# Optimization experiments

Hardware: AMD Instinct MI355X
Metric: run time of the kernel (lower is better)

## Reference

```python
import jax, jax.numpy as jnp
import numpy as np

# Bit index 0 = LSB of the IEEE-754 uint32 pattern (little-endian bit order):
# bits[..., 0:23] mantissa, bits[..., 23:31] exponent, bits[..., 31] sign.
_SHIFTS = jnp.arange(32, dtype=jnp.uint32)


def f32_to_bits(x):
    """float32 [...] -> pulse bits [..., 32] in {0., 1.}."""
    u = jax.lax.bitcast_convert_type(x, jnp.uint32)
    return ((u[..., None] >> _SHIFTS) & jnp.uint32(1)).astype(jnp.float32)


def bits_to_f32(b):
    """pulse bits [..., 32] -> float32 [...]. Exact inverse of f32_to_bits."""
    u = jnp.sum(b.astype(jnp.uint32) << _SHIFTS, axis=-1, dtype=jnp.uint32)
    return jax.lax.bitcast_convert_type(u, jnp.float32)


def setup_inputs() -> dict:
    key = jax.random.key(0)
    kA, kB = jax.random.split(key)
    # Encode realistic fp32 values into pulse (bit) tensors.
    A_vals = jax.random.normal(kA, (4, 512, 512), dtype=jnp.float32)   # [B, M, K]
    B_vals = jax.random.normal(kB, (512, 512), dtype=jnp.float32)      # [K, N]
    return {"A": f32_to_bits(A_vals), "B": f32_to_bits(B_vals)}


def reference(A, B):
    """Spike-domain FP32 matmul: decode pulses -> fp32 GEMM -> re-encode pulses.

    A: [..., M, K, 32] pulses, B: [K, N, 32] pulses -> C: [..., M, N, 32] pulses.
    The spiking multiplier/adder gates implement exact IEEE-754 fp32 multiply
    and sequential accumulation over k, i.e. C[..., i, j] = sum_k A[...,i,k]*B[k,j]
    in fp32.
    """
    A_f = bits_to_f32(A)                         # [B, M, K]
    B_f = bits_to_f32(B)                         # [K, N]
    C = jnp.einsum('bmk,kn->bmn', A_f, B_f)      # fp32 accumulation
    return f32_to_bits(C)                        # [B, M, N, 32]
```

## Files before the change

### kernel.cpp

```cpp
#include <hip/hip_runtime.h>
#include <stdint.h>

#define BATCH 4
#define MDIM  512
#define KDIM  512
#define NDIM  512
#define ROWS  (BATCH * MDIM)
#define BR    4
#define BCOLS 256

#define WORDS_A (ROWS * KDIM)
#define WORDS_B (KDIM * NDIM)
#define WORDS_T (WORDS_A + WORDS_B)
#define DEC_BLOCKS 2048
#define DEC_WAVES  (DEC_BLOCKS * 4)
#define DEC_ITERS  (WORDS_T / (32 * DEC_WAVES))

__device__ __forceinline__ uint32_t spread4(uint32_t x) {
    x = (x | (x << 12)) & 0x000F000Fu;
    x = (x | (x << 6))  & 0x03030303u;
    x = (x | (x << 3))  & 0x11111111u;
    return x;
}

__global__ __launch_bounds__(256) void decode_all(const float* __restrict__ Abits,
                                                  const float* __restrict__ Bbits,
                                                  uint32_t* __restrict__ Au,
                                                  uint32_t* __restrict__ Bu) {
    const int lane = threadIdx.x & 63;
    const int waveId = (blockIdx.x * blockDim.x + threadIdx.x) >> 6;
    const int sh = lane & 56;

#pragma unroll
    for (int i = 0; i < DEC_ITERS; ++i) {
        const int wb = (waveId + i * DEC_WAVES) * 32;
        const float* src;
        uint32_t* dst;
        if (wb < WORDS_A) { src = Abits + (size_t)wb * 32;             dst = Au + wb; }
        else              { src = Bbits + (size_t)(wb - WORDS_A) * 32; dst = Bu + (wb - WORDS_A); }

        uint4 v0 = ((const uint4*)src)[lane];
        uint4 v1 = ((const uint4*)src)[lane + 64];
        uint4 v2 = ((const uint4*)src)[lane + 128];
        uint4 v3 = ((const uint4*)src)[lane + 192];

        unsigned long long m[16];
        m[0]  = __ballot((v0.x >> 29) & 1u);
        m[1]  = __ballot((v0.y >> 29) & 1u);
        m[2]  = __ballot((v0.z >> 29) & 1u);
        m[3]  = __ballot((v0.w >> 29) & 1u);
        m[4]  = __ballot((v1.x >> 29) & 1u);
        m[5]  = __ballot((v1.y >> 29) & 1u);
        m[6]  = __ballot((v1.z >> 29) & 1u);
        m[7]  = __ballot((v1.w >> 29) & 1u);
        m[8]  = __ballot((v2.x >> 29) & 1u);
        m[9]  = __ballot((v2.y >> 29) & 1u);
        m[10] = __ballot((v2.z >> 29) & 1u);
        m[11] = __ballot((v2.w >> 29) & 1u);
        m[12] = __ballot((v3.x >> 29) & 1u);
        m[13] = __ballot((v3.y >> 29) & 1u);
        m[14] = __ballot((v3.z >> 29) & 1u);
        m[15] = __ballot((v3.w >> 29) & 1u);

        if ((lane & 7) == 0) {
#pragma unroll
            for (int g = 0; g < 4; ++g) {
                uint32_t w = (spread4((uint32_t)(m[4*g+0] >> sh) & 0xFFu) << 0)
                           | (spread4((uint32_t)(m[4*g+1] >> sh) & 0xFFu) << 1)
                           | (spread4((uint32_t)(m[4*g+2] >> sh) & 0xFFu) << 2)
                           | (spread4((uint32_t)(m[4*g+3] >> sh) & 0xFFu) << 3);
                dst[8 * g + (lane >> 3)] = w;
            }
        }
    }
}

__global__ __launch_bounds__(256) void gemm_encode(const float* __restrict__ A,
                                                   const float* __restrict__ B,
                                                   float* __restrict__ outbits) {
    __shared__ uint32_t Us[BR][BCOLS];

    const int tid = threadIdx.x;
    const int rowBase = blockIdx.x * BR;
    const int n0 = blockIdx.y * BCOLS;
    const int n = n0 + tid;

    float acc[BR];
#pragma unroll
    for (int r = 0; r < BR; ++r) acc[r] = 0.0f;

    const float* Bcol = B + n;
    const float* Arow = A + (size_t)rowBase * KDIM;

    float bn[8], bc[8];
#pragma unroll
    for (int i = 0; i < 8; ++i) bn[i] = Bcol[(size_t)i * NDIM];

#pragma unroll 2
    for (int k0 = 0; k0 < KDIM; k0 += 8) {
#pragma unroll
        for (int i = 0; i < 8; ++i) bc[i] = bn[i];
        const int kp = (k0 + 8) & (KDIM - 1);
#pragma unroll
        for (int i = 0; i < 8; ++i) bn[i] = Bcol[(size_t)(kp + i) * NDIM];

        float4 a0[BR], a1[BR];
#pragma unroll
        for (int r = 0; r < BR; ++r) {
            a0[r] = *(const float4*)(Arow + (size_t)r * KDIM + k0);
            a1[r] = *(const float4*)(Arow + (size_t)r * KDIM + k0 + 4);
        }
#pragma unroll
        for (int r = 0; r < BR; ++r) {
            acc[r] = __builtin_fmaf(a0[r].x, bc[0], acc[r]);
            acc[r] = __builtin_fmaf(a0[r].y, bc[1], acc[r]);
            acc[r] = __builtin_fmaf(a0[r].z, bc[2], acc[r]);
            acc[r] = __builtin_fmaf(a0[r].w, bc[3], acc[r]);
            acc[r] = __builtin_fmaf(a1[r].x, bc[4], acc[r]);
            acc[r] = __builtin_fmaf(a1[r].y, bc[5], acc[r]);
            acc[r] = __builtin_fmaf(a1[r].z, bc[6], acc[r]);
            acc[r] = __builtin_fmaf(a1[r].w, bc[7], acc[r]);
        }
    }

#pragma unroll
    for (int r = 0; r < BR; ++r) Us[r][tid] = __float_as_uint(acc[r]);
    __syncthreads();

    float* oBase = outbits + ((size_t)rowBase * NDIM + n0) * 32;
    const int b = (tid & 7) * 4;
#pragma unroll
    for (int r = 0; r < BR; ++r) {
        float* o = oBase + (size_t)r * NDIM * 32;
#pragma unroll
        for (int it = 0; it < 8; ++it) {
            uint32_t u = Us[r][it * 32 + (tid >> 3)];
            float4 q;
            q.x = (float)((u >> (b + 0)) & 1u);
            q.y = (float)((u >> (b + 1)) & 1u);
            q.z = (float)((u >> (b + 2)) & 1u);
            q.w = (float)((u >> (b + 3)) & 1u);
            *(float4*)(o + it * 1024 + tid * 4) = q;
        }
    }
}

extern "C" void kernel_launch(void* const* d_in, const int* in_sizes, int n_in,
                              void* d_out, int out_size, void* d_ws, size_t ws_size,
                              hipStream_t stream) {
    const float* Abits = (const float*)d_in[0];
    const float* Bbits = (const float*)d_in[1];
    float* out = (float*)d_out;

    uint32_t* A_u = (uint32_t*)d_ws;
    uint32_t* B_u = A_u + WORDS_A;

    decode_all<<<DEC_BLOCKS, 256, 0, stream>>>(Abits, Bbits, A_u, B_u);

    dim3 grid(ROWS / BR, NDIM / BCOLS);
    gemm_encode<<<grid, 256, 0, stream>>>((const float*)A_u, (const float*)B_u, out);
}
```

Measured before the change: 83.84 us.

## Fuse A pulse decoding into GEMM kernel via shared memory, widen block to full N

The decode of A's bit tensor moves into the GEMM kernel. Each 512-thread block decodes its 4-row A panel straight into shared memory and then computes all 512 output columns. This removes the round trip of writing the decoded A words to global memory and reading them back, and A is decoded once per row panel rather than being read by two column blocks. Only B is still decoded by a separate kernel. The cost is fewer blocks (512 instead of 1024) and a decode phase inside each block that has to finish before the FMA loop can start.

```diff
diff --git a/kernel.cpp b/kernel.cpp
--- a/kernel.cpp
+++ b/kernel.cpp
@@ -7,14 +7,9 @@
 #define NDIM  512
 #define ROWS  (BATCH * MDIM)
 #define BR    4
-#define BCOLS 256
+#define THREADS 512
 
-#define WORDS_A (ROWS * KDIM)
 #define WORDS_B (KDIM * NDIM)
-#define WORDS_T (WORDS_A + WORDS_B)
-#define DEC_BLOCKS 2048
-#define DEC_WAVES  (DEC_BLOCKS * 4)
-#define DEC_ITERS  (WORDS_T / (32 * DEC_WAVES))
 
 __device__ __forceinline__ uint32_t spread4(uint32_t x) {
     x = (x | (x << 12)) & 0x000F000Fu;
@@ -23,74 +18,93 @@
     return x;
 }
 
-__global__ __launch_bounds__(256) void decode_all(const float* __restrict__ Abits,
-                                                  const float* __restrict__ Bbits,
-                                                  uint32_t* __restrict__ Au,
-                                                  uint32_t* __restrict__ Bu) {
+__global__ __launch_bounds__(256) void decode_B(const float* __restrict__ Bbits,
+                                                uint32_t* __restrict__ Bu) {
     const int lane = threadIdx.x & 63;
     const int waveId = (blockIdx.x * blockDim.x + threadIdx.x) >> 6;
     const int sh = lane & 56;
 
+    const int wb = waveId * 32;
+    const float* src = Bbits + (size_t)wb * 32;
+    uint32_t* dst = Bu + wb;
+
+    uint4 v0 = ((const uint4*)src)[lane];
+    uint4 v1 = ((const uint4*)src)[lane + 64];
+    uint4 v2 = ((const uint4*)src)[lane + 128];
+    uint4 v3 = ((const uint4*)src)[lane + 192];
+
+    unsigned long long m[16];
+    m[0]  = __ballot((v0.x >> 29) & 1u);  m[1]  = __ballot((v0.y >> 29) & 1u);
+    m[2]  = __ballot((v0.z >> 29) & 1u);  m[3]  = __ballot((v0.w >> 29) & 1u);
+    m[4]  = __ballot((v1.x >> 29) & 1u);  m[5]  = __ballot((v1.y >> 29) & 1u);
+    m[6]  = __ballot((v1.z >> 29) & 1u);  m[7]  = __ballot((v1.w >> 29) & 1u);
+    m[8]  = __ballot((v2.x >> 29) & 1u);  m[9]  = __ballot((v2.y >> 29) & 1u);
+    m[10] = __ballot((v2.z >> 29) & 1u);  m[11] = __ballot((v2.w >> 29) & 1u);
+    m[12] = __ballot((v3.x >> 29) & 1u);  m[13] = __ballot((v3.y >> 29) & 1u);
+    m[14] = __ballot((v3.z >> 29) & 1u);  m[15] = __ballot((v3.w >> 29) & 1u);
+
+    if ((lane & 7) == 0) {
 #pragma unroll
-    for (int i = 0; i < DEC_ITERS; ++i) {
-        const int wb = (waveId + i * DEC_WAVES) * 32;
-        const float* src;
-        uint32_t* dst;
-        if (wb < WORDS_A) { src = Abits + (size_t)wb * 32;             dst = Au + wb; }
-        else              { src = Bbits + (size_t)(wb - WORDS_A) * 32; dst = Bu + (wb - WORDS_A); }
+        for (int q = 0; q < 4; ++q) {
+            uint32_t w = (spread4((uint32_t)(m[4*q+0] >> sh) & 0xFFu) << 0)
+                       | (spread4((uint32_t)(m[4*q+1] >> sh) & 0xFFu) << 1)
+                       | (spread4((uint32_t)(m[4*q+2] >> sh) & 0xFFu) << 2)
+                       | (spread4((uint32_t)(m[4*q+3] >> sh) & 0xFFu) << 3);
+            dst[8 * q + (lane >> 3)] = w;
+        }
+    }
+}
 
+__global__ __launch_bounds__(THREADS) void gemm_fused(const float* __restrict__ Abits,
+                                                      const float* __restrict__ Bu,
+                                                      float* __restrict__ outbits) {
+    __shared__ uint32_t AsU[BR][KDIM];
+
+    const int tid  = threadIdx.x;
+    const int lane = tid & 63;
+    const int wv   = tid >> 6;
+    const int rowBase = blockIdx.x * BR;
+    const int sh = lane & 56;
+
+    const float* panel = Abits + (size_t)rowBase * KDIM * 32;
+#pragma unroll
+    for (int i = 0; i < 8; ++i) {
+        const float* src = panel + wv * 8192 + i * 1024;
         uint4 v0 = ((const uint4*)src)[lane];
         uint4 v1 = ((const uint4*)src)[lane + 64];
         uint4 v2 = ((const uint4*)src)[lane + 128];
         uint4 v3 = ((const uint4*)src)[lane + 192];
 
         unsigned long long m[16];
-        m[0]  = __ballot((v0.x >> 29) & 1u);
-        m[1]  = __ballot((v0.y >> 29) & 1u);
-        m[2]  = __ballot((v0.z >> 29) & 1u);
-        m[3]  = __ballot((v0.w >> 29) & 1u);
-        m[4]  = __ballot((v1.x >> 29) & 1u);
-        m[5]  = __ballot((v1.y >> 29) & 1u);
-        m[6]  = __ballot((v1.z >> 29) & 1u);
-        m[7]  = __ballot((v1.w >> 29) & 1u);
-        m[8]  = __ballot((v2.x >> 29) & 1u);
-        m[9]  = __ballot((v2.y >> 29) & 1u);
-        m[10] = __ballot((v2.z >> 29) & 1u);
-        m[11] = __ballot((v2.w >> 29) & 1u);
-        m[12] = __ballot((v3.x >> 29) & 1u);
-        m[13] = __ballot((v3.y >> 29) & 1u);
-        m[14] = __ballot((v3.z >> 29) & 1u);
-        m[15] = __ballot((v3.w >> 29) & 1u);
+        m[0]  = __ballot((v0.x >> 29) & 1u);  m[1]  = __ballot((v0.y >> 29) & 1u);
+        m[2]  = __ballot((v0.z >> 29) & 1u);  m[3]  = __ballot((v0.w >> 29) & 1u);
+        m[4]  = __ballot((v1.x >> 29) & 1u);  m[5]  = __ballot((v1.y >> 29) & 1u);
+        m[6]  = __ballot((v1.z >> 29) & 1u);  m[7]  = __ballot((v1.w >> 29) & 1u);
+        m[8]  = __ballot((v2.x >> 29) & 1u);  m[9]  = __ballot((v2.y >> 29) & 1u);
+        m[10] = __ballot((v2.z >> 29) & 1u);  m[11] = __ballot((v2.w >> 29) & 1u);
+        m[12] = __ballot((v3.x >> 29) & 1u);  m[13] = __ballot((v3.y >> 29) & 1u);
+        m[14] = __ballot((v3.z >> 29) & 1u);  m[15] = __ballot((v3.w >> 29) & 1u);
 
         if ((lane & 7) == 0) {
 #pragma unroll
-            for (int g = 0; g < 4; ++g) {
-                uint32_t w = (spread4((uint32_t)(m[4*g+0] >> sh) & 0xFFu) << 0)
-                           | (spread4((uint32_t)(m[4*g+1] >> sh) & 0xFFu) << 1)
-                           | (spread4((uint32_t)(m[4*g+2] >> sh) & 0xFFu) << 2)
-                           | (spread4((uint32_t)(m[4*g+3] >> sh) & 0xFFu) << 3);
-                dst[8 * g + (lane >> 3)] = w;
+            for (int q = 0; q < 4; ++q) {
+                uint32_t w = (spread4((uint32_t)(m[4*q+0] >> sh) & 0xFFu) << 0)
+                           | (spread4((uint32_t)(m[4*q+1] >> sh) & 0xFFu) << 1)
+                           | (spread4((uint32_t)(m[4*q+2] >> sh) & 0xFFu) << 2)
+                           | (spread4((uint32_t)(m[4*q+3] >> sh) & 0xFFu) << 3);
+                int wi = wv * 256 + i * 32 + q * 8 + (lane >> 3);
+                AsU[wi >> 9][wi & (KDIM - 1)] = w;
             }
         }
     }
-}
-
-__global__ __launch_bounds__(256) void gemm_encode(const float* __restrict__ A,
-                                                   const float* __restrict__ B,
-                                                   float* __restrict__ outbits) {
-    __shared__ uint32_t Us[BR][BCOLS];
-
-    const int tid = threadIdx.x;
-    const int rowBase = blockIdx.x * BR;
-    const int n0 = blockIdx.y * BCOLS;
-    const int n = n0 + tid;
+    __syncthreads();
 
     float acc[BR];
 #pragma unroll
     for (int r = 0; r < BR; ++r) acc[r] = 0.0f;
 
-    const float* Bcol = B + n;
-    const float* Arow = A + (size_t)rowBase * KDIM;
+    const float* Bcol = (const float*)Bu + tid;
+    const float* Asf = (const float*)&AsU[0][0];
 
     float bn[8], bc[8];
 #pragma unroll
@@ -107,8 +121,8 @@
         float4 a0[BR], a1[BR];
 #pragma unroll
         for (int r = 0; r < BR; ++r) {
-            a0[r] = *(const float4*)(Arow + (size_t)r * KDIM + k0);
-            a1[r] = *(const float4*)(Arow + (size_t)r * KDIM + k0 + 4);
+            a0[r] = *(const float4*)(Asf + r * KDIM + k0);
+            a1[r] = *(const float4*)(Asf + r * KDIM + k0 + 4);
         }
 #pragma unroll
         for (int r = 0; r < BR; ++r) {
@@ -122,25 +136,27 @@
             acc[r] = __builtin_fmaf(a1[r].w, bc[7], acc[r]);
         }
     }
-
-#pragma unroll
-    for (int r = 0; r < BR; ++r) Us[r][tid] = __float_as_uint(acc[r]);
     __syncthreads();
 
-    float* oBase = outbits + ((size_t)rowBase * NDIM + n0) * 32;
+    uint32_t* Us = &AsU[0][0];
+#pragma unroll
+    for (int r = 0; r < BR; ++r) Us[r * NDIM + tid] = __float_as_uint(acc[r]);
+    __syncthreads();
+
+    float* oBase = outbits + (size_t)rowBase * NDIM * 32;
     const int b = (tid & 7) * 4;
 #pragma unroll
     for (int r = 0; r < BR; ++r) {
         float* o = oBase + (size_t)r * NDIM * 32;
 #pragma unroll
         for (int it = 0; it < 8; ++it) {
-            uint32_t u = Us[r][it * 32 + (tid >> 3)];
+            uint32_t u = Us[r * NDIM + it * 64 + (tid >> 3)];
             float4 q;
             q.x = (float)((u >> (b + 0)) & 1u);
             q.y = (float)((u >> (b + 1)) & 1u);
             q.z = (float)((u >> (b + 2)) & 1u);
             q.w = (float)((u >> (b + 3)) & 1u);
-            *(float4*)(o + it * 1024 + tid * 4) = q;
+            *(float4*)(o + it * 2048 + tid * 4) = q;
         }
     }
 }
@@ -152,11 +168,8 @@
     const float* Bbits = (const float*)d_in[1];
     float* out = (float*)d_out;
 
-    uint32_t* A_u = (uint32_t*)d_ws;
-    uint32_t* B_u = A_u + WORDS_A;
+    uint32_t* B_u = (uint32_t*)d_ws;
 
-    decode_all<<<DEC_BLOCKS, 256, 0, stream>>>(Abits, Bbits, A_u, B_u);
-
-    dim3 grid(ROWS / BR, NDIM / BCOLS);
-    gemm_encode<<<grid, 256, 0, stream>>>((const float*)A_u, (const float*)B_u, out);
+    decode_B<<<2048, 256, 0, stream>>>(Bbits, B_u);
+    gemm_fused<<<ROWS / BR, THREADS, 0, stream>>>(Abits, (const float*)B_u, out);
 }
```

Result: no change. 82.86 us (-1.2%).
